# Kernel tuning notes

Hardware: AMD Instinct MI355X
Metric: run time of the kernel (lower is better)

## Reference

```python
import jax, jax.numpy as jnp
import numpy as np

B = 131072   # batch of cells
D = 128      # input_dim == number of per-node models
OUTDIM = 2   # predict_var=True -> (delta, var) heads per node


def setup_inputs() -> dict:
    key = jax.random.key(0)
    k1, k2, k3 = jax.random.split(key, 3)
    state = jax.random.normal(k1, (B, D), dtype=jnp.float32)
    # Stacked weights of the D tiny Linear(D, 2) layers: W[n] is node n's [2, D] weight
    W = jax.random.normal(k2, (D, OUTDIM, D), dtype=jnp.float32) * 0.05
    b = jax.random.normal(k3, (D, OUTDIM), dtype=jnp.float32) * 0.05
    return {"state": state, "W": W, "b": b}


def reference(state, W, b):
    # Original: for each node i, y = Linear_i(state) -> delta[:, i] = y[:, 0]; var[:, i] = y[:, 1]
    # Batched equivalent: one einsum over all nodes at once.
    out = jnp.einsum('bd,nod->bno', state, W) + b  # [B, D, 2]
    delta = out[:, :, 0]
    var = out[:, :, 1]
    return delta, var
```

## Files before the change

kernel.cpp:

```cpp
#include <hip/hip_runtime.h>

typedef __attribute__((ext_vector_type(8))) short bf16x8;
typedef __attribute__((ext_vector_type(4))) float f32x4;

constexpr int BROWS = 131072;
constexpr int DDIM  = 128;
constexpr int NTILES = BROWS / 16;
constexpr int CLSBLOCKS = 2048;
constexpr int ITERS = NTILES / CLSBLOCKS;

__device__ __forceinline__ short to_bf16(float f) {
    unsigned u = __builtin_bit_cast(unsigned, f);
    u = (u + 0x7FFFu + ((u >> 16) & 1u)) >> 16;
    return (short)u;
}

__device__ __forceinline__ bf16x8 cvt8(f32x4 lo, f32x4 hi) {
    bf16x8 r;
#pragma unroll
    for (int i = 0; i < 4; ++i) { r[i] = to_bf16(lo[i]); r[i + 4] = to_bf16(hi[i]); }
    return r;
}

__global__ void __launch_bounds__(256, 4)
lfm_kernel(const float* __restrict__ state, const float* __restrict__ W,
           const float* __restrict__ bias, float* __restrict__ out) {
    const int lane = threadIdx.x & 63;
    const int wave = threadIdx.x >> 6;
    const int l16  = lane & 15;
    const int lq   = lane >> 4;

    const int cls = blockIdx.x & 1;
    const int tb  = blockIdx.x >> 1;
    const int colbase = wave * 32;

    bf16x8 wfrag[2][4];
    f32x4  bias4[2];
#pragma unroll
    for (int ct = 0; ct < 2; ++ct) {
        const int n = colbase + ct * 16 + l16;
        const float* wrow = W + n * 256 + cls * 128;
#pragma unroll
        for (int ks = 0; ks < 4; ++ks) {
            f32x4 lo = *reinterpret_cast<const f32x4*>(wrow + ks * 32 + lq * 8);
            f32x4 hi = *reinterpret_cast<const f32x4*>(wrow + ks * 32 + lq * 8 + 4);
            wfrag[ct][ks] = cvt8(lo, hi);
        }
        const int c0 = colbase + ct * 16 + lq * 4;
#pragma unroll
        for (int r = 0; r < 4; ++r)
            bias4[ct][r] = bias[(c0 + r) * 2 + cls];
    }

    float* oplane = out + (size_t)cls * BROWS * 128;

#define LOADT(BUF, T) { \
    const float* srow = state + ((size_t)((T) * 16 + l16)) * DDIM + lq * 8; \
    _Pragma("unroll") \
    for (int ks = 0; ks < 4; ++ks) { \
        BUF[2 * ks]     = *reinterpret_cast<const f32x4*>(srow + ks * 32); \
        BUF[2 * ks + 1] = *reinterpret_cast<const f32x4*>(srow + ks * 32 + 4); \
    } }

#define COMPUTE(BUF, T) { \
    f32x4 acc0 = bias4[0], acc1 = bias4[1]; \
    _Pragma("unroll") \
    for (int ks = 0; ks < 4; ++ks) { \
        bf16x8 af = cvt8(BUF[2 * ks], BUF[2 * ks + 1]); \
        acc0 = __builtin_amdgcn_mfma_f32_16x16x32_bf16(wfrag[0][ks], af, acc0, 0, 0, 0); \
        acc1 = __builtin_amdgcn_mfma_f32_16x16x32_bf16(wfrag[1][ks], af, acc1, 0, 0, 0); \
    } \
    float* orow = oplane + ((size_t)((T) * 16 + l16)) * 128; \
    *reinterpret_cast<f32x4*>(orow + colbase + lq * 4)      = acc0; \
    *reinterpret_cast<f32x4*>(orow + colbase + 16 + lq * 4) = acc1; }

    f32x4 rawA[8], rawB[8];
    LOADT(rawA, tb)
    LOADT(rawB, (tb + CLSBLOCKS))
    COMPUTE(rawA, tb)
    LOADT(rawA, (tb + 2 * CLSBLOCKS))
    COMPUTE(rawB, (tb + CLSBLOCKS))
    LOADT(rawB, (tb + 3 * CLSBLOCKS))
    COMPUTE(rawA, (tb + 2 * CLSBLOCKS))
    COMPUTE(rawB, (tb + 3 * CLSBLOCKS))
#undef LOADT
#undef COMPUTE
}

extern "C" void kernel_launch(void* const* d_in, const int* in_sizes, int n_in,
                              void* d_out, int out_size, void* d_ws, size_t ws_size,
                              hipStream_t stream) {
    const float* state = (const float*)d_in[0];
    const float* W     = (const float*)d_in[1];
    const float* bias  = (const float*)d_in[2];
    float* out = (float*)d_out;
    hipLaunchKernelGGL(lfm_kernel, dim3(2 * CLSBLOCKS), dim3(256), 0, stream,
                       state, W, bias, out);
}
```

Baseline: 251.9 us.

## Merge delta/var blocks into 512-thread blocks, deepen pipeline, nontemporal stores

Each block now has eight waves, four per output head, so the delta and var waves of one block read the same state rows. Before, two separate blocks loaded those rows. The grid halves to 1024 blocks, and each block runs eight tiles through a double-buffered load/compute chain instead of four. Output stores become nontemporal so the large write stream does not pollute cache. Fewer resident blocks and a longer serial chain per block may lower latency hiding.

```diff
diff --git a/kernel.cpp b/kernel.cpp
--- a/kernel.cpp
+++ b/kernel.cpp
@@ -3,11 +3,11 @@
 typedef __attribute__((ext_vector_type(8))) short bf16x8;
 typedef __attribute__((ext_vector_type(4))) float f32x4;
 
-constexpr int BROWS = 131072;
-constexpr int DDIM  = 128;
+constexpr int BROWS  = 131072;
+constexpr int DDIM   = 128;
 constexpr int NTILES = BROWS / 16;
-constexpr int CLSBLOCKS = 2048;
-constexpr int ITERS = NTILES / CLSBLOCKS;
+constexpr int GRID   = 1024;
+constexpr int TPB    = NTILES / GRID;
 
 __device__ __forceinline__ short to_bf16(float f) {
     unsigned u = __builtin_bit_cast(unsigned, f);
@@ -22,7 +22,7 @@
     return r;
 }
 
-__global__ void __launch_bounds__(256, 4)
+__global__ void __launch_bounds__(512, 4)
 lfm_kernel(const float* __restrict__ state, const float* __restrict__ W,
            const float* __restrict__ bias, float* __restrict__ out) {
     const int lane = threadIdx.x & 63;
@@ -30,9 +30,8 @@
     const int l16  = lane & 15;
     const int lq   = lane >> 4;
 
-    const int cls = blockIdx.x & 1;
-    const int tb  = blockIdx.x >> 1;
-    const int colbase = wave * 32;
+    const int cls     = wave >> 2;
+    const int colbase = (wave & 3) * 32;
 
     bf16x8 wfrag[2][4];
     f32x4  bias4[2];
@@ -71,18 +70,21 @@
         acc1 = __builtin_amdgcn_mfma_f32_16x16x32_bf16(wfrag[1][ks], af, acc1, 0, 0, 0); \
     } \
     float* orow = oplane + ((size_t)((T) * 16 + l16)) * 128; \
-    *reinterpret_cast<f32x4*>(orow + colbase + lq * 4)      = acc0; \
-    *reinterpret_cast<f32x4*>(orow + colbase + 16 + lq * 4) = acc1; }
+    __builtin_nontemporal_store(acc0, reinterpret_cast<f32x4*>(orow + colbase + lq * 4)); \
+    __builtin_nontemporal_store(acc1, reinterpret_cast<f32x4*>(orow + colbase + 16 + lq * 4)); }
 
+    const int tb = blockIdx.x;
     f32x4 rawA[8], rawB[8];
     LOADT(rawA, tb)
-    LOADT(rawB, (tb + CLSBLOCKS))
-    COMPUTE(rawA, tb)
-    LOADT(rawA, (tb + 2 * CLSBLOCKS))
-    COMPUTE(rawB, (tb + CLSBLOCKS))
-    LOADT(rawB, (tb + 3 * CLSBLOCKS))
-    COMPUTE(rawA, (tb + 2 * CLSBLOCKS))
-    COMPUTE(rawB, (tb + 3 * CLSBLOCKS))
+    LOADT(rawB, (tb + GRID))
+    COMPUTE(rawA, tb)                 LOADT(rawA, (tb + 2 * GRID))
+    COMPUTE(rawB, (tb + GRID))        LOADT(rawB, (tb + 3 * GRID))
+    COMPUTE(rawA, (tb + 2 * GRID))    LOADT(rawA, (tb + 4 * GRID))
+    COMPUTE(rawB, (tb + 3 * GRID))    LOADT(rawB, (tb + 5 * GRID))
+    COMPUTE(rawA, (tb + 4 * GRID))    LOADT(rawA, (tb + 6 * GRID))
+    COMPUTE(rawB, (tb + 5 * GRID))    LOADT(rawB, (tb + 7 * GRID))
+    COMPUTE(rawA, (tb + 6 * GRID))
+    COMPUTE(rawB, (tb + 7 * GRID))
 #undef LOADT
 #undef COMPUTE
 }
@@ -94,6 +96,6 @@
     const float* W     = (const float*)d_in[1];
     const float* bias  = (const float*)d_in[2];
     float* out = (float*)d_out;
-    hipLaunchKernelGGL(lfm_kernel, dim3(2 * CLSBLOCKS), dim3(256), 0, stream,
+    hipLaunchKernelGGL(lfm_kernel, dim3(GRID), dim3(512), 0, stream,
                        state, W, bias, out);
 }
```

After: 269.7 us. 1.07x slower.
